# Optimization experiments

Measured on AMD Instinct MI355X. Metric: run time of the kernel, lower is better.

Reference implementation:

```python
import jax, jax.numpy as jnp
import numpy as np

B, S, HS = 2, 2048, 1024
H, KV, DH = 16, 4, 64
G = H // KV          # GQA group size
EPS = 1e-6
SCALE = DH ** -0.5


def rms_norm(x, w, eps=EPS):
    # normalize in fp32 over last dim, then rescale (matches MTPRMSNorm)
    xf = x.astype(jnp.float32)
    var = jnp.mean(xf * xf, axis=-1, keepdims=True)
    return (w * (xf * jax.lax.rsqrt(var + eps))).astype(x.dtype)


def setup_inputs() -> dict:
    key = jax.random.key(0)
    ks = jax.random.split(key, 6)
    return {
        "hidden_states": jax.random.normal(ks[0], (B, S, HS), jnp.float32),
        "attention_mask": jnp.zeros((1, 1, S, S), jnp.float32),
        "wq": jax.random.normal(ks[1], (HS, H * DH), jnp.float32) * 0.02,
        "wk": jax.random.normal(ks[2], (HS, KV * DH), jnp.float32) * 0.02,
        "wv": jax.random.normal(ks[3], (HS, KV * DH), jnp.float32) * 0.02,
        "wo": jax.random.normal(ks[4], (H * DH, HS), jnp.float32) * 0.02,
        "q_norm_w": jnp.ones((DH,), jnp.float32),
        "k_norm_w": jnp.ones((DH,), jnp.float32),
    }


def reference(hidden_states, attention_mask, wq, wk, wv, wo, q_norm_w, k_norm_w):
    b, s, _ = hidden_states.shape
    # projections -> per-head layout; GQA handled by broadcasting (no repeat)
    q = rms_norm((hidden_states @ wq).reshape(b, s, KV, G, DH), q_norm_w)  # [b,s,kv,g,dh]
    k = rms_norm((hidden_states @ wk).reshape(b, s, KV, DH), k_norm_w)     # [b,s,kv,dh]
    v = (hidden_states @ wv).reshape(b, s, KV, DH)                          # [b,s,kv,dh]

    # scores: [b, kv, g, q, k]
    scores = jnp.einsum("bqhgd,bkhd->bhgqk", q, k) * SCALE
    scores = scores + attention_mask[:, :, None]  # mask broadcasts over (kv,g)
    probs = jax.nn.softmax(scores.astype(jnp.float32), axis=-1).astype(q.dtype)

    out = jnp.einsum("bhgqk,bkhd->bqhgd", probs, v)  # [b,s,kv,g,dh]
    out = out.reshape(b, s, H * DH)
    return out @ wo
```

## Files before the change

kernel.cpp:

```cpp
#include <hip/hip_runtime.h>
#include <hip/hip_bf16.h>


typedef __attribute__((ext_vector_type(8))) short short8_t;
typedef __attribute__((ext_vector_type(4))) float f32x4_t;

__device__ __forceinline__ unsigned short f2bf_bits(float x) {
  unsigned int u = __float_as_uint(x);
  unsigned int r = u + 0x7fff + ((u >> 16) & 1);
  return (unsigned short)(r >> 16);
}
__device__ __forceinline__ float bf2f_bits(unsigned short b) {
  return __uint_as_float(((unsigned int)b) << 16);
}
__device__ __forceinline__ unsigned int cvt_pk_bf16(float lo, float hi) {
  unsigned int r;
  asm("v_cvt_pk_bf16_f32 %0, %1, %2" : "=v"(r) : "v"(lo), "v"(hi));
  return r;
}

__device__ __forceinline__ void async16(void* lds, const void* g) {
  __builtin_amdgcn_global_load_lds(
      (const __attribute__((address_space(1))) void*)g,
      (__attribute__((address_space(3))) void*)lds, 16, 0, 0);
}

__global__ __launch_bounds__(256) void prep(
    const float* __restrict__ hidden, unsigned short* __restrict__ Xbf,
    const float* __restrict__ wq, const float* __restrict__ wk,
    const float* __restrict__ wv, const float* __restrict__ wo,
    unsigned short* __restrict__ Wqkvt, unsigned short* __restrict__ Wot,
    const float* __restrict__ mask, int* __restrict__ flags, float* __restrict__ tmax) {
  __shared__ unsigned short T[64][72];
  const int tid = threadIdx.x;
  int blk = blockIdx.x;
  if (blk < 4096) {
    int i = (blk * 256 + tid) * 4;
    float4 v = *(const float4*)(hidden + i);
    ushort4 o;
    o.x = f2bf_bits(v.x); o.y = f2bf_bits(v.y);
    o.z = f2bf_bits(v.z); o.w = f2bf_bits(v.w);
    *(ushort4*)(Xbf + i) = o;
    return;
  }
  if (blk < 4736) {
    int b = blk - 4096;
    const float* W; unsigned short* Wt; int Nsrc, n_off, bx, by;
    if (b < 256)      { W = wq; Wt = Wqkvt; Nsrc = 1024; n_off = 0;    bx = b & 15;         by = b >> 4; }
    else if (b < 320) { W = wk; Wt = Wqkvt; Nsrc = 256;  n_off = 1024; bx = (b - 256) & 3;  by = (b - 256) >> 2; }
    else if (b < 384) { W = wv; Wt = Wqkvt; Nsrc = 256;  n_off = 1280; bx = (b - 320) & 3;  by = (b - 320) >> 2; }
    else              { W = wo; Wt = Wot;   Nsrc = 1024; n_off = 0;    bx = (b - 384) & 15; by = (b - 384) >> 4; }
    const int tn = bx * 64, tk = by * 64;
    for (int e = tid; e < 4096; e += 256) {
      int kk = e >> 6, nn = e & 63;
      T[nn][kk] = f2bf_bits(W[(size_t)(tk + kk) * Nsrc + tn + nn]);
    }
    __syncthreads();
    for (int e = tid; e < 4096; e += 256) {
      int nn = e >> 6, kk = e & 63;
      Wt[(size_t)(n_off + tn + nn) * 1024 + tk + kk] = T[nn][kk];
    }
    return;
  }
  {
    int mb = blk - 4736;
    const int bx = mb & 31, by = mb >> 5;
    const int bq = by * 64, bk = bx * 64, w = tid >> 6;
    bool nz = false;
    float vmax = -INFINITY;
    #pragma unroll
    for (int i = 0; i < 4; ++i) {
      int e = (i * 256 + tid) * 4;
      int r = e >> 6, c = e & 63;
      float4 v = *(const float4*)(mask + (size_t)(bq + r) * 2048 + bk + c);
      nz |= (v.x != 0.f) | (v.y != 0.f) | (v.z != 0.f) | (v.w != 0.f);
      vmax = fmaxf(vmax, fmaxf(fmaxf(v.x, v.y), fmaxf(v.z, v.w)));
    }
    #pragma unroll
    for (int m = 1; m < 64; m <<= 1) vmax = fmaxf(vmax, __shfl_xor(vmax, m, 64));
    unsigned long long anynz = __ballot((int)nz);
    __shared__ float wm[4];
    __shared__ int wf[4];
    if ((tid & 63) == 0) { wm[w] = vmax; wf[w] = (anynz != 0ull); }
    __syncthreads();
    if (tid == 0) {
      int idx = by * 32 + bx;
      flags[idx] = wf[0] | wf[1] | wf[2] | wf[3];
      tmax[idx] = fmaxf(fmaxf(wm[0], wm[1]), fmaxf(wm[2], wm[3]));
    }
  }
}

__global__ __launch_bounds__(256) void transpose_v(
    const unsigned short* __restrict__ qkv, unsigned short* __restrict__ vt) {
  __shared__ unsigned short T[64][72];
  const int tid = threadIdx.x;
  const int st = blockIdx.x * 64, bk = blockIdx.y;
  const int b = bk >> 2, kvh = bk & 3;
  const unsigned short* src = qkv + (size_t)(b * 2048 + st) * 1536 + 1280 + kvh * 64;
  for (int e = tid; e < 4096; e += 256) {
    int s = e >> 6, d = e & 63;
    T[d][s] = src[(size_t)s * 1536 + d];
  }
  __syncthreads();
  unsigned short* dst = vt + (size_t)bk * 64 * 2048 + st;
  for (int e = tid; e < 4096; e += 256) {
    int d = e >> 6, s = e & 63;
    int p = ((s >> 5) << 5) | (((s >> 2) & 3) << 3) | (((s >> 4) & 1) << 2) | (s & 3);
    dst[(size_t)d * 2048 + p] = T[d][s];
  }
}

template <bool OUT_BF16, bool QKNORM>
__global__ __launch_bounds__(256) void gemm_bt(
    const unsigned short* __restrict__ A, const unsigned short* __restrict__ Bt,
    void* __restrict__ Cp, int M, int N, int K, int ldc,
    const float* __restrict__ qw, const float* __restrict__ kw) {
  __shared__ unsigned short As[64 * 64];
  __shared__ unsigned short Bs[128 * 64];
  const int tid = threadIdx.x;
  const int w = tid >> 6, l = tid & 63, lr = l & 15, lg = l >> 4;
  const int nwg = gridDim.x * gridDim.y;
  int orig = blockIdx.y * gridDim.x + blockIdx.x;
  int wgid = ((nwg & 7) == 0) ? ((orig & 7) * (nwg >> 3) + (orig >> 3)) : orig;
  const int bm = (wgid / gridDim.x) * 64, bn = (wgid % gridDim.x) * 128;
  const int wrow = (w >> 1) * 32, wcol = (w & 1) * 64;

  const int rthr = tid >> 3;
  const int qsw = (tid & 7) ^ (rthr & 7);
  const unsigned short* srcA[2];
  const unsigned short* srcB[4];
  #pragma unroll
  for (int it = 0; it < 2; ++it)
    srcA[it] = A + (size_t)(bm + it * 32 + rthr) * K + qsw * 8;
  #pragma unroll
  for (int it = 0; it < 4; ++it)
    srcB[it] = Bt + (size_t)(bn + it * 32 + rthr) * K + qsw * 8;

  const int c0 = ((lg) ^ (lr & 7)) * 8;
  const int c1 = ((4 + lg) ^ (lr & 7)) * 8;
  const unsigned short* aB[2] = { As + (wrow + lr) * 64 + c0, As + (wrow + lr) * 64 + c1 };
  const unsigned short* bB[2] = { Bs + (wcol + lr) * 64 + c0, Bs + (wcol + lr) * 64 + c1 };

  f32x4_t acc[2][4] = {};

  for (int k0 = 0; k0 < K; k0 += 64) {
    __syncthreads();
    #pragma unroll
    for (int it = 0; it < 2; ++it) {
      async16(As + it * 2048 + w * 512, srcA[it]);
      srcA[it] += 64;
    }
    #pragma unroll
    for (int it = 0; it < 4; ++it) {
      async16(Bs + it * 2048 + w * 512, srcB[it]);
      srcB[it] += 64;
    }
    __syncthreads();
    #pragma unroll
    for (int kd = 0; kd < 2; ++kd) {
      short8_t af[2], bfr[4];
      #pragma unroll
      for (int m = 0; m < 2; ++m)
        af[m] = *(const short8_t*)(aB[kd] + m * 1024);
      #pragma unroll
      for (int n = 0; n < 4; ++n)
        bfr[n] = *(const short8_t*)(bB[kd] + n * 1024);
      #pragma unroll
      for (int m = 0; m < 2; ++m)
        #pragma unroll
        for (int n = 0; n < 4; ++n)
          acc[m][n] = __builtin_amdgcn_mfma_f32_16x16x32_bf16(af[m], bfr[n], acc[m][n], 0, 0, 0);
    }
  }

  if constexpr (QKNORM) {
    int seg = (bn + wcol) >> 6;
    if (seg < 20) {
      const float* wseg = (seg < 16) ? qw : kw;
      float wv[4];
      #pragma unroll
      for (int n = 0; n < 4; ++n) {
        wv[n] = wseg[n * 16 + lr];
        if (seg < 16) wv[n] *= 0.125f;
      }
      #pragma unroll
      for (int m = 0; m < 2; ++m)
        #pragma unroll
        for (int j = 0; j < 4; ++j) {
          float ss = acc[m][0][j] * acc[m][0][j];
          #pragma unroll
          for (int n = 1; n < 4; ++n) ss += acc[m][n][j] * acc[m][n][j];
          #pragma unroll
          for (int x = 1; x < 16; x <<= 1) ss += __shfl_xor(ss, x, 64);
          float rinv = rsqrtf(ss * (1.0f / 64.0f) + 1e-6f);
          #pragma unroll
          for (int n = 0; n < 4; ++n) acc[m][n][j] *= rinv * wv[n];
        }
    }
  }

  #pragma unroll
  for (int m = 0; m < 2; ++m)
    #pragma unroll
    for (int n = 0; n < 4; ++n)
      #pragma unroll
      for (int j = 0; j < 4; ++j) {
        int row = bm + wrow + m * 16 + lg * 4 + j;
        int col = bn + wcol + n * 16 + lr;
        float v = acc[m][n][j];
        if (OUT_BF16) ((unsigned short*)Cp)[(size_t)row * ldc + col] = f2bf_bits(v);
        else          ((float*)Cp)[(size_t)row * ldc + col] = v;
      }
}

__global__ __launch_bounds__(256, 4) void flash_attn(
    const unsigned short* __restrict__ qkv, const unsigned short* __restrict__ vtg,
    const float* __restrict__ mask, const int* __restrict__ flags,
    const float* __restrict__ tmax, const float* __restrict__ qw,
    const float* __restrict__ kw, unsigned short* __restrict__ O) {
  int orig = blockIdx.y * 32 + blockIdx.x;
  int swz = (orig & 7) * 128 + (orig >> 3);
  const int qt = swz & 31, bh = swz >> 5;
  const int b = bh >> 4, hq = bh & 15, kvh = hq >> 2;
  const int tid = threadIdx.x, w = tid >> 6, l = tid & 63, lr = l & 15, lg = l >> 4;

  __shared__ unsigned short Ks[2][64 * 64];
  __shared__ unsigned short Vs[2][64 * 64];

  const unsigned short* Qg = qkv + (size_t)(b * 2048 + qt * 64) * 1536 + hq * 64;
  const unsigned short* Kg = qkv + (size_t)(b * 2048) * 1536 + 1024 + kvh * 64;
  const unsigned short* Vg = vtg + (size_t)(b * 4 + kvh) * 64 * 2048;
  const float* Mg = mask + (size_t)(qt * 64) * 2048;
  const int* Fp = flags + qt * 32;

  auto stage = [&](int kt2, int bi) {
    #pragma unroll
    for (int it = 0; it < 2; ++it) {
      int c = it * 256 + tid;
      int r = c >> 3, cc = (c & 7) ^ (r & 7);
      async16(&Ks[bi][it * 2048 + w * 512],
              Kg + (size_t)(kt2 * 64 + r) * 1536 + cc * 8);
      async16(&Vs[bi][it * 2048 + w * 512],
              Vg + (size_t)r * 2048 + kt2 * 64 + cc * 8);
    }
  };

  stage(0, 0);

  const float L2E = 1.44269504f;
  float pmax = fabsf(qw[l] * kw[l]);
  #pragma unroll
  for (int m = 1; m < 64; m <<= 1) pmax = fmaxf(pmax, __shfl_xor(pmax, m, 64));
  float tmx = (l < 32) ? tmax[qt * 32 + l] : -INFINITY;
  #pragma unroll
  for (int m = 1; m < 64; m <<= 1) tmx = fmaxf(tmx, __shfl_xor(tmx, m, 64));
  const float nm = -(8.0f * pmax + fmaxf(tmx, 0.0f)) * L2E;

  short8_t qf[2];
  {
    const unsigned short* qrow = Qg + (size_t)(w * 16 + lr) * 1536 + lg * 8;
    qf[0] = *(const short8_t*)(qrow);
    qf[1] = *(const short8_t*)(qrow + 32);
  }

  short8_t vb1;
  #pragma unroll
  for (int e = 0; e < 8; ++e) vb1[e] = (lr == 0) ? (short)0x3f80 : (short)0;

  f32x4_t oacc[5] = {};

  for (int kt = 0; kt < 32; ++kt) {
    __syncthreads();
    if (kt < 31) stage(kt + 1, (kt + 1) & 1);
    const int cur = kt & 1;

    f32x4_t sacc[4] = {};
    __builtin_amdgcn_s_setprio(1);
    #pragma unroll
    for (int kd = 0; kd < 2; ++kd)
      #pragma unroll
      for (int n = 0; n < 4; ++n) {
        int kr = n * 16 + lr;
        short8_t kf = *(const short8_t*)(&Ks[cur][kr * 64 + ((kd * 4 + lg) ^ (kr & 7)) * 8]);
        sacc[n] = __builtin_amdgcn_mfma_f32_16x16x32_bf16(kf, qf[kd], sacc[n], 0, 0, 0);
      }
    __builtin_amdgcn_s_setprio(0);

    const bool hasmask = Fp[kt] != 0;
    float e4[4][4];
    #pragma unroll
    for (int n = 0; n < 4; ++n) {
      if (hasmask) {
        float4 mv = *(const float4*)(Mg + (size_t)(w * 16 + lr) * 2048 + kt * 64 + n * 16 + lg * 4);
        e4[n][0] = exp2f(fmaf(sacc[n][0] + mv.x, L2E, nm));
        e4[n][1] = exp2f(fmaf(sacc[n][1] + mv.y, L2E, nm));
        e4[n][2] = exp2f(fmaf(sacc[n][2] + mv.z, L2E, nm));
        e4[n][3] = exp2f(fmaf(sacc[n][3] + mv.w, L2E, nm));
      } else {
        #pragma unroll
        for (int j = 0; j < 4; ++j)
          e4[n][j] = exp2f(fmaf(sacc[n][j], L2E, nm));
      }
    }
    short8_t pa[2];
    #pragma unroll
    for (int kd = 0; kd < 2; ++kd) {
      int4 pk;
      pk.x = (int)cvt_pk_bf16(e4[2 * kd][0],     e4[2 * kd][1]);
      pk.y = (int)cvt_pk_bf16(e4[2 * kd][2],     e4[2 * kd][3]);
      pk.z = (int)cvt_pk_bf16(e4[2 * kd + 1][0], e4[2 * kd + 1][1]);
      pk.w = (int)cvt_pk_bf16(e4[2 * kd + 1][2], e4[2 * kd + 1][3]);
      pa[kd] = *(short8_t*)&pk;
    }

    __builtin_amdgcn_s_setprio(1);
    #pragma unroll
    for (int kd = 0; kd < 2; ++kd) {
      #pragma unroll
      for (int nd = 0; nd < 4; ++nd) {
        int vr = nd * 16 + lr;
        short8_t vb = *(const short8_t*)(&Vs[cur][vr * 64 + ((kd * 4 + lg) ^ (vr & 7)) * 8]);
        oacc[nd] = __builtin_amdgcn_mfma_f32_16x16x32_bf16(pa[kd], vb, oacc[nd], 0, 0, 0);
      }
      oacc[4] = __builtin_amdgcn_mfma_f32_16x16x32_bf16(pa[kd], vb1, oacc[4], 0, 0, 0);
    }
    __builtin_amdgcn_s_setprio(0);
  }

  float rln[4];
  #pragma unroll
  for (int j = 0; j < 4; ++j) rln[j] = 1.0f / __shfl(oacc[4][j], l & 48, 64);
  #pragma unroll
  for (int nd = 0; nd < 4; ++nd)
    #pragma unroll
    for (int j = 0; j < 4; ++j) {
      size_t row = (size_t)(b * 2048 + qt * 64 + w * 16 + lg * 4 + j);
      O[row * 1024 + hq * 64 + nd * 16 + lr] = f2bf_bits(oacc[nd][j] * rln[j]);
    }
}

extern "C" void kernel_launch(void* const* d_in, const int* in_sizes, int n_in,
                              void* d_out, int out_size, void* d_ws, size_t ws_size,
                              hipStream_t stream) {
  const float* hidden = (const float*)d_in[0];
  const float* mask   = (const float*)d_in[1];
  const float* wq     = (const float*)d_in[2];
  const float* wk     = (const float*)d_in[3];
  const float* wv     = (const float*)d_in[4];
  const float* wo     = (const float*)d_in[5];
  const float* qw     = (const float*)d_in[6];
  const float* kw     = (const float*)d_in[7];

  char* ws = (char*)d_ws;
  unsigned short* Xbf   = (unsigned short*)(ws);
  unsigned short* Wqkvt = (unsigned short*)(ws +  8388608);
  unsigned short* Wot   = (unsigned short*)(ws + 11534336);
  unsigned short* QKV   = (unsigned short*)(ws + 13631488);
  unsigned short* Vtg   = Wqkvt;
  unsigned short* Obf   = Xbf;

  char* dtail = (char*)d_out + (size_t)out_size * 4 - 8192;
  int*   flags = (int*)dtail;
  float* tmaxb = (float*)(dtail + 4096);

  prep<<<5760, 256, 0, stream>>>(hidden, Xbf, wq, wk, wv, wo, Wqkvt, Wot, mask, flags, tmaxb);

  gemm_bt<true, true><<<dim3(12, 64), 256, 0, stream>>>(
      Xbf, Wqkvt, QKV, 4096, 1536, 1024, 1536, qw, kw);
  transpose_v<<<dim3(32, 8), 256, 0, stream>>>(QKV, Vtg);
  flash_attn<<<dim3(32, 32), 256, 0, stream>>>(QKV, Vtg, mask, flags, tmaxb, qw, kw, Obf);
  gemm_bt<false, false><<<dim3(8, 64), 256, 0, stream>>>(
      Obf, Wot, d_out, 4096, 1024, 1024, 1024, nullptr, nullptr);
}
```

Measured before the change: 120.0 us.

## Double-buffer LDS tiles in gemm_bt to overlap global loads with MFMA

Splits the shared-memory A and B tiles into two buffers. The kernel now prefetches the next K-slice with async global-to-LDS loads while MFMAs run on the current slice, which removes one barrier per iteration. The change aims to hide global memory latency in the projection GEMMs. In exchange it doubles LDS use per block, which may reduce occupancy, and it relies on the barrier draining the outstanding async loads.

```diff
diff --git a/kernel.cpp b/kernel.cpp
--- a/kernel.cpp
+++ b/kernel.cpp
@@ -116,8 +116,8 @@
     const unsigned short* __restrict__ A, const unsigned short* __restrict__ Bt,
     void* __restrict__ Cp, int M, int N, int K, int ldc,
     const float* __restrict__ qw, const float* __restrict__ kw) {
-  __shared__ unsigned short As[64 * 64];
-  __shared__ unsigned short Bs[128 * 64];
+  __shared__ unsigned short As[2][64 * 64];
+  __shared__ unsigned short Bs[2][128 * 64];
   const int tid = threadIdx.x;
   const int w = tid >> 6, l = tid & 63, lr = l & 15, lg = l >> 4;
   const int nwg = gridDim.x * gridDim.y;
@@ -137,35 +137,41 @@
   for (int it = 0; it < 4; ++it)
     srcB[it] = Bt + (size_t)(bn + it * 32 + rthr) * K + qsw * 8;
 
-  const int c0 = ((lg) ^ (lr & 7)) * 8;
-  const int c1 = ((4 + lg) ^ (lr & 7)) * 8;
-  const unsigned short* aB[2] = { As + (wrow + lr) * 64 + c0, As + (wrow + lr) * 64 + c1 };
-  const unsigned short* bB[2] = { Bs + (wcol + lr) * 64 + c0, Bs + (wcol + lr) * 64 + c1 };
+  auto stage = [&](int bi) {
+    #pragma unroll
+    for (int it = 0; it < 2; ++it) {
+      async16(&As[bi][it * 2048 + w * 512], srcA[it]);
+      srcA[it] += 64;
+    }
+    #pragma unroll
+    for (int it = 0; it < 4; ++it) {
+      async16(&Bs[bi][it * 2048 + w * 512], srcB[it]);
+      srcB[it] += 64;
+    }
+  };
+
+  stage(0);
 
   f32x4_t acc[2][4] = {};
-
-  for (int k0 = 0; k0 < K; k0 += 64) {
+  const int nst = K >> 6;
+
+  for (int st = 0; st < nst; ++st) {
     __syncthreads();
-    #pragma unroll
-    for (int it = 0; it < 2; ++it) {
-      async16(As + it * 2048 + w * 512, srcA[it]);
-      srcA[it] += 64;
-    }
-    #pragma unroll
-    for (int it = 0; it < 4; ++it) {
-      async16(Bs + it * 2048 + w * 512, srcB[it]);
-      srcB[it] += 64;
-    }
-    __syncthreads();
+    if (st + 1 < nst) stage((st + 1) & 1);
+    const int cur = st & 1;
     #pragma unroll
     for (int kd = 0; kd < 2; ++kd) {
       short8_t af[2], bfr[4];
       #pragma unroll
-      for (int m = 0; m < 2; ++m)
-        af[m] = *(const short8_t*)(aB[kd] + m * 1024);
-      #pragma unroll
-      for (int n = 0; n < 4; ++n)
-        bfr[n] = *(const short8_t*)(bB[kd] + n * 1024);
+      for (int m = 0; m < 2; ++m) {
+        int r = wrow + m * 16 + lr;
+        af[m] = *(const short8_t*)(&As[cur][r * 64 + ((kd * 4 + lg) ^ (r & 7)) * 8]);
+      }
+      #pragma unroll
+      for (int n = 0; n < 4; ++n) {
+        int r = wcol + n * 16 + lr;
+        bfr[n] = *(const short8_t*)(&Bs[cur][r * 64 + ((kd * 4 + lg) ^ (r & 7)) * 8]);
+      }
       #pragma unroll
       for (int m = 0; m < 2; ++m)
         #pragma unroll
```

After: 118.8 us. No clear change (-1.0%).
